# Kernel optimization log

Measured on AMD Instinct MI355X. Metric: run time of the kernel, lower is better.

Reference implementation:

```python
import jax, jax.numpy as jnp
import numpy as np

M_FACTORS = [12, 8, 8]
N_FACTORS = [8, 8, 12]
E = 4          # hardcoded in original: gates.view(B, 4, 1, 1, 1)
R = 8          # TT rank
ALPHA = 16.0   # common_alpha
TAU = 1.0


def setup_inputs() -> dict:
    key = jax.random.key(0)
    ks = jax.random.split(key, 11)
    B, S, m = 32, 512, 768
    inp = {
        "X": jax.random.normal(ks[0], (B, S, m), jnp.float32),
        "router_w": jax.random.normal(ks[1], (E, m), jnp.float32) * 0.02,
        "router_b": jax.random.normal(ks[2], (E,), jnp.float32) * 0.02,
        "base_w": jax.random.normal(ks[3], (m, m), jnp.float32) * 0.02,
        "base_b": jax.random.normal(ks[4], (m,), jnp.float32) * 0.02,
        "core0": jax.random.normal(ks[5], (E, 1, 12, R), jnp.float32) * 0.1,
        "core1": jax.random.normal(ks[6], (E, R, 8, R), jnp.float32) * 0.1,
        "core2": jax.random.normal(ks[7], (E, R, 8, R), jnp.float32) * 0.1,
        "core3": jax.random.normal(ks[8], (E, R, 8, R), jnp.float32) * 0.1,
        "core4": jax.random.normal(ks[9], (E, R, 8, R), jnp.float32) * 0.1,
        "core5": jax.random.normal(ks[10], (E, R, 12, 1), jnp.float32) * 0.1,
    }
    return inp


def _gumbel_softmax_hard(logits, key):
    # torch.nn.functional.gumbel_softmax(logits, tau=TAU, hard=True)
    u = jax.random.uniform(key, logits.shape, logits.dtype, 1e-6, 1.0 - 1e-6)
    g = -jnp.log(-jnp.log(u))
    y_soft = jax.nn.softmax((logits + g) / TAU, axis=-1)
    y_hard = jax.nn.one_hot(jnp.argmax(y_soft, axis=-1), logits.shape[-1],
                            dtype=logits.dtype)
    # straight-through: y_hard - sg(y_soft) + y_soft
    return jax.lax.stop_gradient(y_hard - y_soft) + y_soft


def _tt_moe(X, gates, cores):
    # faithful to tensorized_multiplication_experts
    B, S, m = X.shape
    # [B, 1, S, m_factors[::-1]] -> last axis is m_factors[0]
    tt_state = X.reshape([B, 1, S] + M_FACTORS[::-1])
    num_m = len(M_FACTORS)
    for i in range(num_m):
        # per-sample expert-weighted core: [B, r, f, p]
        mc = jnp.einsum('be,erfp->brfp', gates, cores[i])
        tt_state = jnp.einsum('br...m,brmp->bp...', tt_state, mc)
    for i in range(len(N_FACTORS)):
        mc = jnp.einsum('be,erfp->brfp', gates, cores[num_m + i])
        tt_state = jnp.einsum('br...,brnp->bp...n', tt_state, mc)
    return tt_state.reshape(B, S, -1)  # trailing p == 1


def reference(X, router_w, router_b, base_w, base_b,
              core0, core1, core2, core3, core4, core5):
    cores = [core0, core1, core2, core3, core4, core5]
    pooled = X.mean(axis=1)                              # [B, m]
    logits = pooled @ router_w.T + router_b              # [B, E]
    gates = _gumbel_softmax_hard(logits, jax.random.key(42))
    base_out = X @ base_w.T + base_b                     # F.linear
    Z = _tt_moe(X, gates, cores)                         # [B, S, n]
    return Z * ALPHA + base_out
```

## Files before the change

### kernel.cpp

```cpp
#include <hip/hip_runtime.h>
#include <hip/hip_bf16.h>
#include <stdint.h>

#define GAS __attribute__((address_space(1)))
#define LAS __attribute__((address_space(3)))

typedef __attribute__((ext_vector_type(8))) short bf16x8;
typedef __attribute__((ext_vector_type(4))) float f32x4;

struct us4 { unsigned short x, y, z, w; };

__device__ __forceinline__ void gl_lds16(const void* g, void* lds) {
  __builtin_amdgcn_global_load_lds((const GAS unsigned int*)(uintptr_t)g,
                                   (LAS unsigned int*)(uintptr_t)lds, 16, 0, 0);
}

__device__ __forceinline__ unsigned short f2bf(float f) {
  unsigned u = __float_as_uint(f);
  return (unsigned short)((u + 0x7fffu + ((u >> 16) & 1u)) >> 16);
}

__device__ __forceinline__ void threefry2x32_42(unsigned x0, unsigned x1,
                                                unsigned* o0, unsigned* o1) {
  const unsigned k0 = 0u, k1 = 42u;
  unsigned ks[3] = {k0, k1, k0 ^ k1 ^ 0x1BD11BDAu};
  x0 += ks[0]; x1 += ks[1];
  const int rot[2][4] = {{13, 15, 26, 6}, {17, 29, 16, 24}};
#pragma unroll
  for (int i = 0; i < 5; ++i) {
#pragma unroll
    for (int j = 0; j < 4; ++j) {
      int r = rot[i & 1][j];
      x0 += x1;
      x1 = (x1 << r) | (x1 >> (32 - r));
      x1 ^= x0;
    }
    x0 += ks[(i + 1) % 3];
    x1 += ks[(i + 2) % 3] + (unsigned)(i + 1);
  }
  *o0 = x0; *o1 = x1;
}

__global__ __launch_bounds__(256) void k_prep(
    const float* __restrict__ X, const float* __restrict__ rw,
    const float* __restrict__ bw,
    const float* __restrict__ c0, const float* __restrict__ c1,
    const float* __restrict__ c2, const float* __restrict__ c3,
    const float* __restrict__ c4, const float* __restrict__ c5,
    unsigned short* __restrict__ Xbf, float* __restrict__ partial,
    unsigned short* __restrict__ Wbt) {
  __shared__ __align__(16) char smem[31232];
  int t = threadIdx.x;
  int bid = blockIdx.x;

  if (bid < 192) {
    int e = bid / 48, jc = bid % 48;
    float* KA = (float*)smem;
    float* LB = (float*)(smem + 3072);
    float* Kt = (float*)(smem + 6144);
    float* LtS = (float*)(smem + 30720);
    for (int q = t; q < 768; q += 256) {
      int bc = q >> 3, p2 = q & 7;
      int b2 = bc / 12, cc = bc % 12;
      float s = 0.f;
#pragma unroll
      for (int p1 = 0; p1 < 8; ++p1)
        s += c0[e * 96 + cc * 8 + p1] * c1[((e * 8 + p1) * 8 + b2) * 8 + p2];
      KA[q] = s;
      int p4 = q / 96, mm = q % 96;
      int n2 = mm / 12, n3 = mm % 12;
      float s2 = 0.f;
#pragma unroll
      for (int p5 = 0; p5 < 8; ++p5)
        s2 += c4[((e * 8 + p4) * 8 + n2) * 8 + p5] * c5[(e * 8 + p5) * 12 + n3];
      LB[q] = s2;
    }
    __syncthreads();
    for (int q = t; q < 6144; q += 256) {
      int i = q >> 3, p3 = q & 7;
      int a = i / 96, bc = i % 96;
      float s = 0.f;
#pragma unroll
      for (int p2 = 0; p2 < 8; ++p2)
        s += KA[bc * 8 + p2] * c2[((e * 8 + p2) * 8 + a) * 8 + p3];
      Kt[p3 * 768 + i] = s;
    }
    if (t < 128) {
      int i = t >> 3, p3 = t & 7;
      int j = jc * 16 + i;
      int n1 = j / 96, mm = j % 96;
      float s2 = 0.f;
#pragma unroll
      for (int p4 = 0; p4 < 8; ++p4)
        s2 += c3[((e * 8 + p3) * 8 + n1) * 8 + p4] * LB[p4 * 96 + mm];
      LtS[i * 8 + p3] = s2;
    }
    __syncthreads();
    for (int idx = t; idx < 12288; idx += 256) {
      int jl = idx / 768, i = idx - jl * 768;
      int j = jc * 16 + jl;
      float s = 0.f;
#pragma unroll
      for (int p = 0; p < 8; ++p) s += Kt[p * 768 + i] * LtS[jl * 8 + p];
      float val = bw[(size_t)j * 768 + i] + 16.0f * s;
      Wbt[(size_t)e * 589824 + (size_t)j * 768 + i] = f2bf(val);
    }
  } else {
    float* red = (float*)smem;
    int p = bid - 192;
    int r0 = p * 32;
    float lp0 = 0.f, lp1 = 0.f, lp2 = 0.f, lp3 = 0.f;
    if (t < 192) {
      const float* xp = X + (size_t)r0 * 768 + t * 4;
      unsigned short* xo = Xbf + (size_t)r0 * 768 + t * 4;
      float4 acc = {0.f, 0.f, 0.f, 0.f};
#pragma unroll 8
      for (int r = 0; r < 32; ++r) {
        float4 v = *reinterpret_cast<const float4*>(xp + (size_t)r * 768);
        acc.x += v.x; acc.y += v.y; acc.z += v.z; acc.w += v.w;
        us4 o;
        o.x = f2bf(v.x); o.y = f2bf(v.y); o.z = f2bf(v.z); o.w = f2bf(v.w);
        *reinterpret_cast<us4*>(xo + (size_t)r * 768) = o;
      }
      float4 w0 = *reinterpret_cast<const float4*>(rw + 0 * 768 + t * 4);
      float4 w1 = *reinterpret_cast<const float4*>(rw + 1 * 768 + t * 4);
      float4 w2 = *reinterpret_cast<const float4*>(rw + 2 * 768 + t * 4);
      float4 w3 = *reinterpret_cast<const float4*>(rw + 3 * 768 + t * 4);
      lp0 = acc.x * w0.x + acc.y * w0.y + acc.z * w0.z + acc.w * w0.w;
      lp1 = acc.x * w1.x + acc.y * w1.y + acc.z * w1.z + acc.w * w1.w;
      lp2 = acc.x * w2.x + acc.y * w2.y + acc.z * w2.z + acc.w * w2.w;
      lp3 = acc.x * w3.x + acc.y * w3.y + acc.z * w3.z + acc.w * w3.w;
    }
#pragma unroll
    for (int off = 32; off > 0; off >>= 1) {
      lp0 += __shfl_down(lp0, off);
      lp1 += __shfl_down(lp1, off);
      lp2 += __shfl_down(lp2, off);
      lp3 += __shfl_down(lp3, off);
    }
    int w = t >> 6;
    if ((t & 63) == 0 && w < 3) {
      red[w * 4 + 0] = lp0; red[w * 4 + 1] = lp1;
      red[w * 4 + 2] = lp2; red[w * 4 + 3] = lp3;
    }
    __syncthreads();
    if (t < 4) partial[p * 4 + t] = red[0 + t] + red[4 + t] + red[8 + t];
  }
}

__global__ __launch_bounds__(256, 4) void k_gemm(
    const unsigned short* __restrict__ Xbf,
    const unsigned short* __restrict__ Wbt,
    const float* __restrict__ partial,
    const float* __restrict__ rb,
    const float* __restrict__ base_b,
    float* __restrict__ out)
{
  __shared__ unsigned short sA[128 * 64];
  __shared__ unsigned short sB[96 * 64];
  int t = threadIdx.x;
  int w = t >> 6, l = t & 63;
  int l16 = l & 15, l4 = l >> 4;

  int bid = blockIdx.x;
  int work = (bid & 7) * 128 + (bid >> 3);
  int mtile = work >> 3, ntile = work & 7;
  int m0 = mtile * 128, n0 = ntile * 96;
  int b = mtile >> 2;

  int bi = 0;
  {
    float v = -1e30f;
    if (l < 4) {
      float s = 0.f;
#pragma unroll
      for (int c = 0; c < 16; ++c) s += partial[(b * 16 + c) * 4 + l];
      float lg = s * (1.0f / 512.0f) + rb[l];
      int idx = b * 4 + l;
      unsigned x0, x1;
      threefry2x32_42(0u, (unsigned)idx, &x0, &x1);
      unsigned bits = x0 ^ x1;
      float u01 = __uint_as_float((bits >> 9) | 0x3f800000u) - 1.0f;
      float u = u01 * ((1.0f - 1e-6f) - 1e-6f) + 1e-6f;
      u = fmaxf(u, 1e-6f);
      v = lg + (-logf(-logf(u)));
      bi = l;
#pragma unroll
      for (int off = 1; off < 4; off <<= 1) {
        float vo = __shfl_xor(v, off);
        int io = __shfl_xor(bi, off);
        if (vo > v || (vo == v && io < bi)) { v = vo; bi = io; }
      }
    }
    bi = __shfl(bi, 0);
  }
  const unsigned short* Wb = Wbt + (size_t)bi * 589824;
  int wr = w & 1, wc = w >> 1;

  f32x4 acc[4][3];
#pragma unroll
  for (int i = 0; i < 4; ++i)
#pragma unroll
    for (int jj = 0; jj < 3; ++jj) acc[i][jj] = (f32x4)0.f;

  int arow[4], acsw[4];
#pragma unroll
  for (int q = 0; q < 4; ++q) {
    int ci = (w * 4 + q) * 64 + l;
    arow[q] = ci >> 3;
    acsw[q] = ((ci & 7) * 8) ^ ((arow[q] & 7) << 3);
  }
  int brow[3], bcsw[3];
#pragma unroll
  for (int q = 0; q < 3; ++q) {
    int ci = (w * 3 + q) * 64 + l;
    brow[q] = ci >> 3;
    bcsw[q] = ((ci & 7) * 8) ^ ((brow[q] & 7) << 3);
  }

  int xorr = (l16 & 7) << 3;
  for (int k0 = 0; k0 < 768; k0 += 64) {
#pragma unroll
    for (int q = 0; q < 4; ++q) {
      const unsigned short* ga = Xbf + (size_t)(m0 + arow[q]) * 768 + k0 + acsw[q];
      gl_lds16(ga, &sA[(w * 4 + q) * 512]);
    }
#pragma unroll
    for (int q = 0; q < 3; ++q) {
      const unsigned short* gb = Wb + (size_t)(n0 + brow[q]) * 768 + k0 + bcsw[q];
      gl_lds16(gb, &sB[(w * 3 + q) * 512]);
    }
    __syncthreads();
#pragma unroll
    for (int kk = 0; kk < 2; ++kk) {
      int coff = (kk * 32 + l4 * 8) ^ xorr;
      bf16x8 af[4], bfr[3];
#pragma unroll
      for (int am = 0; am < 4; ++am)
        af[am] = *reinterpret_cast<const bf16x8*>(
            &sA[(wr * 64 + am * 16 + l16) * 64 + coff]);
#pragma unroll
      for (int bn = 0; bn < 3; ++bn)
        bfr[bn] = *reinterpret_cast<const bf16x8*>(
            &sB[(wc * 48 + bn * 16 + l16) * 64 + coff]);
#pragma unroll
      for (int am = 0; am < 4; ++am)
#pragma unroll
        for (int bn = 0; bn < 3; ++bn)
          acc[am][bn] = __builtin_amdgcn_mfma_f32_16x16x32_bf16(
              bfr[bn], af[am], acc[am][bn], 0, 0, 0);
    }
    __syncthreads();
  }

  f32x4 bb4[3];
#pragma unroll
  for (int bn = 0; bn < 3; ++bn)
    bb4[bn] = *reinterpret_cast<const f32x4*>(base_b + n0 + wc * 48 + bn * 16 + l4 * 4);
#pragma unroll
  for (int am = 0; am < 4; ++am) {
    int m = m0 + wr * 64 + am * 16 + l16;
    float* op = out + (size_t)m * 768 + n0 + wc * 48 + l4 * 4;
#pragma unroll
    for (int bn = 0; bn < 3; ++bn) {
      f32x4 v = acc[am][bn] + bb4[bn];
      *reinterpret_cast<f32x4*>(op + bn * 16) = v;
    }
  }
}

extern "C" void kernel_launch(void* const* d_in, const int* in_sizes, int n_in,
                              void* d_out, int out_size, void* d_ws, size_t ws_size,
                              hipStream_t stream) {
  const float* X  = (const float*)d_in[0];
  const float* rw = (const float*)d_in[1];
  const float* rb = (const float*)d_in[2];
  const float* bw = (const float*)d_in[3];
  const float* bb = (const float*)d_in[4];
  const float* c0 = (const float*)d_in[5];
  const float* c1 = (const float*)d_in[6];
  const float* c2 = (const float*)d_in[7];
  const float* c3 = (const float*)d_in[8];
  const float* c4 = (const float*)d_in[9];
  const float* c5 = (const float*)d_in[10];
  float* out = (float*)d_out;

  char* ws = (char*)d_ws;
  float* partial      = (float*)(ws + 4096);
  unsigned short* Wbt = (unsigned short*)(ws + 262144);
  unsigned short* Xbf = (unsigned short*)(ws + 4980736);

  k_prep<<<704, 256, 0, stream>>>(X, rw, bw, c0, c1, c2, c3, c4, c5,
                                  Xbf, partial, Wbt);
  k_gemm<<<1024, 256, 0, stream>>>(Xbf, Wbt, partial, rb, bb, out);
}
```

Before: 56.56 us.

## Double-buffer LDS tiles in GEMM to overlap global loads with MFMA

Splits the shared-memory A/B tiles into two buffers and prefetches the next K-slice with direct global-to-LDS loads while the current slice feeds the MFMAs, dropping one barrier per iteration. The aim is to hide global load latency behind compute. LDS per block doubles to about 56 KB and the launch-bounds occupancy hint drops from 4 to 2 blocks per CU, so fewer resident waves are available to hide latency in other ways.

New measurement: 57.55 us. No clear change (+1.8%).

```diff
diff --git a/kernel.cpp b/kernel.cpp
--- a/kernel.cpp
+++ b/kernel.cpp
@@ -148,7 +148,7 @@
   }
 }
 
-__global__ __launch_bounds__(256, 4) void k_gemm(
+__global__ __launch_bounds__(256, 2) void k_gemm(
     const unsigned short* __restrict__ Xbf,
     const unsigned short* __restrict__ Wbt,
     const float* __restrict__ partial,
@@ -156,8 +156,8 @@
     const float* __restrict__ base_b,
     float* __restrict__ out)
 {
-  __shared__ unsigned short sA[128 * 64];
-  __shared__ unsigned short sB[96 * 64];
+  __shared__ unsigned short sA[2][128 * 64];
+  __shared__ unsigned short sB[2][96 * 64];
   int t = threadIdx.x;
   int w = t >> 6, l = t & 63;
   int l16 = l & 15, l4 = l >> 4;
@@ -218,19 +218,27 @@
     bcsw[q] = ((ci & 7) * 8) ^ ((brow[q] & 7) << 3);
   }
 
+#define STAGE(bufi, k0)                                                        \
+  {                                                                            \
+    _Pragma("unroll") for (int q = 0; q < 4; ++q) {                            \
+      const unsigned short* ga =                                               \
+          Xbf + (size_t)(m0 + arow[q]) * 768 + (k0) + acsw[q];                 \
+      gl_lds16(ga, &sA[bufi][(w * 4 + q) * 512]);                              \
+    }                                                                          \
+    _Pragma("unroll") for (int q = 0; q < 3; ++q) {                            \
+      const unsigned short* gb =                                               \
+          Wb + (size_t)(n0 + brow[q]) * 768 + (k0) + bcsw[q];                  \
+      gl_lds16(gb, &sB[bufi][(w * 3 + q) * 512]);                              \
+    }                                                                          \
+  }
+
+  STAGE(0, 0);
+  __syncthreads();
+
   int xorr = (l16 & 7) << 3;
-  for (int k0 = 0; k0 < 768; k0 += 64) {
-#pragma unroll
-    for (int q = 0; q < 4; ++q) {
-      const unsigned short* ga = Xbf + (size_t)(m0 + arow[q]) * 768 + k0 + acsw[q];
-      gl_lds16(ga, &sA[(w * 4 + q) * 512]);
-    }
-#pragma unroll
-    for (int q = 0; q < 3; ++q) {
-      const unsigned short* gb = Wb + (size_t)(n0 + brow[q]) * 768 + k0 + bcsw[q];
-      gl_lds16(gb, &sB[(w * 3 + q) * 512]);
-    }
-    __syncthreads();
+  for (int kt = 0; kt < 12; ++kt) {
+    int cur = kt & 1;
+    if (kt < 11) STAGE(cur ^ 1, (kt + 1) * 64);
 #pragma unroll
     for (int kk = 0; kk < 2; ++kk) {
       int coff = (kk * 32 + l4 * 8) ^ xorr;
@@ -238,11 +246,11 @@
 #pragma unroll
       for (int am = 0; am < 4; ++am)
         af[am] = *reinterpret_cast<const bf16x8*>(
-            &sA[(wr * 64 + am * 16 + l16) * 64 + coff]);
+            &sA[cur][(wr * 64 + am * 16 + l16) * 64 + coff]);
 #pragma unroll
       for (int bn = 0; bn < 3; ++bn)
         bfr[bn] = *reinterpret_cast<const bf16x8*>(
-            &sB[(wc * 48 + bn * 16 + l16) * 64 + coff]);
+            &sB[cur][(wc * 48 + bn * 16 + l16) * 64 + coff]);
 #pragma unroll
       for (int am = 0; am < 4; ++am)
 #pragma unroll
@@ -252,6 +260,7 @@
     }
     __syncthreads();
   }
+#undef STAGE
 
   f32x4 bb4[3];
 #pragma unroll
```

## Apply TT expert as low-rank correction inside GEMM instead of materializing per-expert weights

Applied to the files above, without the earlier changes.

Instead of building four dense 768x768 bf16 weight matrices (base plus each expert's low-rank TT product), the prep kernel now emits only the rank-8 factors K^T and L per expert plus a bf16 copy of base_w. The GEMM computes an extra rank-8 projection X·K with additional MFMAs, then applies the L factor and alpha scaling in the epilogue. This cuts prep work and weight memory traffic (no 4x589824 dense construction). In exchange the GEMM gains extra MFMAs, LDS usage and epilogue FLOPs, and it drops the occupancy hint from launch bounds.

Result: slower. 59.30 us (+4.8%).

```diff
diff --git a/kernel.cpp b/kernel.cpp
--- a/kernel.cpp
+++ b/kernel.cpp
@@ -48,17 +48,16 @@
     const float* __restrict__ c2, const float* __restrict__ c3,
     const float* __restrict__ c4, const float* __restrict__ c5,
     unsigned short* __restrict__ Xbf, float* __restrict__ partial,
-    unsigned short* __restrict__ Wbt) {
-  __shared__ __align__(16) char smem[31232];
+    unsigned short* __restrict__ KmatT, float* __restrict__ Lt,
+    unsigned short* __restrict__ bwt) {
+  __shared__ __align__(16) char smem[8192];
   int t = threadIdx.x;
   int bid = blockIdx.x;
 
-  if (bid < 192) {
-    int e = bid / 48, jc = bid % 48;
+  if (bid < 4) {
+    int e = bid;
     float* KA = (float*)smem;
     float* LB = (float*)(smem + 3072);
-    float* Kt = (float*)(smem + 6144);
-    float* LtS = (float*)(smem + 30720);
     for (int q = t; q < 768; q += 256) {
       int bc = q >> 3, p2 = q & 7;
       int b2 = bc / 12, cc = bc % 12;
@@ -83,31 +82,27 @@
 #pragma unroll
       for (int p2 = 0; p2 < 8; ++p2)
         s += KA[bc * 8 + p2] * c2[((e * 8 + p2) * 8 + a) * 8 + p3];
-      Kt[p3 * 768 + i] = s;
-    }
-    if (t < 128) {
-      int i = t >> 3, p3 = t & 7;
-      int j = jc * 16 + i;
-      int n1 = j / 96, mm = j % 96;
+      KmatT[(size_t)e * 6144 + p3 * 768 + i] = f2bf(s);
+      int n1 = i / 96, mm = i % 96;
       float s2 = 0.f;
 #pragma unroll
       for (int p4 = 0; p4 < 8; ++p4)
         s2 += c3[((e * 8 + p3) * 8 + n1) * 8 + p4] * LB[p4 * 96 + mm];
-      LtS[i * 8 + p3] = s2;
-    }
-    __syncthreads();
-    for (int idx = t; idx < 12288; idx += 256) {
-      int jl = idx / 768, i = idx - jl * 768;
-      int j = jc * 16 + jl;
-      float s = 0.f;
-#pragma unroll
-      for (int p = 0; p < 8; ++p) s += Kt[p * 768 + i] * LtS[jl * 8 + p];
-      float val = bw[(size_t)j * 768 + i] + 16.0f * s;
-      Wbt[(size_t)e * 589824 + (size_t)j * 768 + i] = f2bf(val);
+      Lt[(size_t)e * 6144 + q] = s2;
+    }
+  } else if (bid < 196) {
+    int base = (bid - 4) * 3072;
+#pragma unroll
+    for (int r = 0; r < 3; ++r) {
+      int idx = base + r * 1024 + t * 4;
+      float4 v = *reinterpret_cast<const float4*>(bw + idx);
+      us4 o;
+      o.x = f2bf(v.x); o.y = f2bf(v.y); o.z = f2bf(v.z); o.w = f2bf(v.w);
+      *reinterpret_cast<us4*>(bwt + idx) = o;
     }
   } else {
     float* red = (float*)smem;
-    int p = bid - 192;
+    int p = bid - 196;
     int r0 = p * 32;
     float lp0 = 0.f, lp1 = 0.f, lp2 = 0.f, lp3 = 0.f;
     if (t < 192) {
@@ -148,9 +143,11 @@
   }
 }
 
-__global__ __launch_bounds__(256, 4) void k_gemm(
+__global__ __launch_bounds__(256) void k_gemm(
     const unsigned short* __restrict__ Xbf,
-    const unsigned short* __restrict__ Wbt,
+    const unsigned short* __restrict__ bwt,
+    const unsigned short* __restrict__ KmatT,
+    const float* __restrict__ Lt,
     const float* __restrict__ partial,
     const float* __restrict__ rb,
     const float* __restrict__ base_b,
@@ -158,6 +155,8 @@
 {
   __shared__ unsigned short sA[128 * 64];
   __shared__ unsigned short sB[96 * 64];
+  __shared__ unsigned short sKp[8 * 776];
+  __shared__ float sL[96 * 8];
   int t = threadIdx.x;
   int w = t >> 6, l = t & 63;
   int l16 = l & 15, l4 = l >> 4;
@@ -194,14 +193,25 @@
     }
     bi = __shfl(bi, 0);
   }
-  const unsigned short* Wb = Wbt + (size_t)bi * 589824;
   int wr = w & 1, wc = w >> 1;
 
+#pragma unroll
+  for (int rho = 0; rho < 8; ++rho)
+    if (t < 192)
+      *reinterpret_cast<us4*>(&sKp[rho * 776 + t * 4]) =
+          *reinterpret_cast<const us4*>(&KmatT[(size_t)bi * 6144 + rho * 768 + t * 4]);
+  if (t < 192)
+    *reinterpret_cast<f32x4*>(&sL[t * 4]) =
+        *reinterpret_cast<const f32x4*>(&Lt[(size_t)bi * 6144 + n0 * 8 + t * 4]);
+
   f32x4 acc[4][3];
 #pragma unroll
   for (int i = 0; i < 4; ++i)
 #pragma unroll
     for (int jj = 0; jj < 3; ++jj) acc[i][jj] = (f32x4)0.f;
+  f32x4 acc_y[4];
+#pragma unroll
+  for (int i = 0; i < 4; ++i) acc_y[i] = (f32x4)0.f;
 
   int arow[4], acsw[4];
 #pragma unroll
@@ -219,6 +229,7 @@
   }
 
   int xorr = (l16 & 7) << 3;
+  int krow = (l16 & 7) * 776;
   for (int k0 = 0; k0 < 768; k0 += 64) {
 #pragma unroll
     for (int q = 0; q < 4; ++q) {
@@ -227,7 +238,7 @@
     }
 #pragma unroll
     for (int q = 0; q < 3; ++q) {
-      const unsigned short* gb = Wb + (size_t)(n0 + brow[q]) * 768 + k0 + bcsw[q];
+      const unsigned short* gb = bwt + (size_t)(n0 + brow[q]) * 768 + k0 + bcsw[q];
       gl_lds16(gb, &sB[(w * 3 + q) * 512]);
     }
     __syncthreads();
@@ -243,12 +254,19 @@
       for (int bn = 0; bn < 3; ++bn)
         bfr[bn] = *reinterpret_cast<const bf16x8*>(
             &sB[(wc * 48 + bn * 16 + l16) * 64 + coff]);
+      bf16x8 kfr = *reinterpret_cast<const bf16x8*>(
+          &sKp[krow + k0 + kk * 32 + l4 * 8]);
+      if (l16 >= 8) kfr = (bf16x8)(short)0;
 #pragma unroll
       for (int am = 0; am < 4; ++am)
 #pragma unroll
         for (int bn = 0; bn < 3; ++bn)
           acc[am][bn] = __builtin_amdgcn_mfma_f32_16x16x32_bf16(
               bfr[bn], af[am], acc[am][bn], 0, 0, 0);
+#pragma unroll
+      for (int am = 0; am < 4; ++am)
+        acc_y[am] = __builtin_amdgcn_mfma_f32_16x16x32_bf16(
+            kfr, af[am], acc_y[am], 0, 0, 0);
     }
     __syncthreads();
   }
@@ -259,11 +277,25 @@
     bb4[bn] = *reinterpret_cast<const f32x4*>(base_b + n0 + wc * 48 + bn * 16 + l4 * 4);
 #pragma unroll
   for (int am = 0; am < 4; ++am) {
+    float y[8];
+#pragma unroll
+    for (int r = 0; r < 4; ++r) {
+      y[r]     = __shfl(acc_y[am][r], l16);
+      y[r + 4] = __shfl(acc_y[am][r], l16 + 16);
+    }
     int m = m0 + wr * 64 + am * 16 + l16;
     float* op = out + (size_t)m * 768 + n0 + wc * 48 + l4 * 4;
 #pragma unroll
     for (int bn = 0; bn < 3; ++bn) {
-      f32x4 v = acc[am][bn] + bb4[bn];
+      f32x4 v;
+#pragma unroll
+      for (int r = 0; r < 4; ++r) {
+        int nl = wc * 48 + bn * 16 + l4 * 4 + r;
+        float corr = 0.f;
+#pragma unroll
+        for (int p = 0; p < 8; ++p) corr += y[p] * sL[nl * 8 + p];
+        v[r] = acc[am][bn][r] + bb4[bn][r] + 16.0f * corr;
+      }
       *reinterpret_cast<f32x4*>(op + bn * 16) = v;
     }
   }
@@ -286,11 +318,13 @@
   float* out = (float*)d_out;
 
   char* ws = (char*)d_ws;
-  float* partial      = (float*)(ws + 4096);
-  unsigned short* Wbt = (unsigned short*)(ws + 262144);
-  unsigned short* Xbf = (unsigned short*)(ws + 4980736);
-
-  k_prep<<<704, 256, 0, stream>>>(X, rw, bw, c0, c1, c2, c3, c4, c5,
-                                  Xbf, partial, Wbt);
-  k_gemm<<<1024, 256, 0, stream>>>(Xbf, Wbt, partial, rb, bb, out);
-}
+  float* partial        = (float*)(ws + 4096);
+  unsigned short* KmatT = (unsigned short*)(ws + 65536);
+  float* Lt             = (float*)(ws + 131072);
+  unsigned short* bwt   = (unsigned short*)(ws + 262144);
+  unsigned short* Xbf   = (unsigned short*)(ws + 4980736);
+
+  k_prep<<<708, 256, 0, stream>>>(X, rw, bw, c0, c1, c2, c3, c4, c5,
+                                  Xbf, partial, KmatT, Lt, bwt);
+  k_gemm<<<1024, 256, 0, stream>>>(Xbf, bwt, KmatT, Lt, partial, rb, bb, out);
+}
```
